# Kernel tuning notes

Measured on AMD Instinct MI355X. Metric: run time of the kernel, lower is better.

Reference implementation:

```python
import jax, jax.numpy as jnp
import numpy as np

DIM = 1024
HEADS = 16
DIM_HEAD = DIM // HEADS  # 64
B, N = 4, 1024


def setup_inputs() -> dict:
    key = jax.random.key(0)
    ks = jax.random.split(key, 8)
    s = 1.0 / np.sqrt(DIM)
    inp = {
        "x": jax.random.normal(ks[0], (B, N, DIM), dtype=jnp.float32),
        # weights stored as [in, out] so y = x @ W (+ b), equivalent to torch Linear
        "Wq": jax.random.normal(ks[1], (DIM, DIM), dtype=jnp.float32) * s,
        "Wk": jax.random.normal(ks[2], (DIM, DIM), dtype=jnp.float32) * s,
        "Wv": jax.random.normal(ks[3], (DIM, DIM), dtype=jnp.float32) * s,
        "Wproj": jax.random.normal(ks[4], (DIM, DIM), dtype=jnp.float32) * s,
        "bproj": jnp.zeros((DIM,), dtype=jnp.float32),
        "Wpre": jax.random.normal(ks[5], (DIM, DIM), dtype=jnp.float32) * s,
        "bpre": jnp.zeros((DIM,), dtype=jnp.float32),
        # original init is -inf (non-runnable); use a finite trained value
        "pi": jnp.full((1,), 0.5, dtype=jnp.float32),
    }
    return inp


def reference(x, Wq, Wk, Wv, Wproj, bproj, Wpre, bpre, pi):
    b, n, c = x.shape
    h, dh = HEADS, DIM_HEAD
    residual = x
    # bias-logit path: Linear -> SiLU -> bmm with itself (dropout p=0 is identity)
    pre = jax.nn.silu(x @ Wpre + bpre)                       # [B,N,C]
    logits = jnp.einsum('bnc,bmc->bnm', pre, pre) / jnp.sqrt(jnp.float32(c))
    # QKV (x2 defaults to x)
    q = (x @ Wq).reshape(b, n, h, dh).transpose(0, 2, 1, 3)  # [B,H,N,Dh]
    k = (x @ Wk).reshape(b, n, h, dh).transpose(0, 2, 1, 3)
    v = (x @ Wv).reshape(b, n, h, dh).transpose(0, 2, 1, 3)
    score = jnp.einsum('bhnd,bhmd->bhnm', q, k) / jnp.sqrt(jnp.float32(dh))
    final_logits = pi[0] * logits[:, None, :, :] + score     # broadcast bias over heads
    attn = jax.nn.softmax(final_logits, axis=-1)
    out = jnp.einsum('bhnm,bhmd->bhnd', attn, v)             # [B,H,N,Dh]
    out = out.transpose(0, 2, 1, 3).reshape(b, n, h * dh)
    out = out @ Wproj + bproj
    return out + residual
```

## Files before the change

kernel.cpp:

```cpp
#include <hip/hip_runtime.h>

using bf16x8 = __attribute__((ext_vector_type(8))) short;
using v8bf   = __attribute__((ext_vector_type(8))) __bf16;
using f32x4  = __attribute__((ext_vector_type(4))) float;

typedef const __attribute__((address_space(1))) void GASV;
typedef __attribute__((address_space(3))) void LASV;

template <typename V>
__device__ __forceinline__ auto mfma_bf16_impl(V a, V b, f32x4 c, int)
    -> decltype(__builtin_amdgcn_mfma_f32_16x16x32_bf16(a, b, c, 0, 0, 0)) {
  return __builtin_amdgcn_mfma_f32_16x16x32_bf16(a, b, c, 0, 0, 0);
}
template <typename V>
__device__ __forceinline__ f32x4 mfma_bf16_impl(V a, V b, f32x4 c, long) {
  return __builtin_amdgcn_mfma_f32_16x16x32_bf16(
      __builtin_bit_cast(v8bf, a), __builtin_bit_cast(v8bf, b), c, 0, 0, 0);
}
__device__ __forceinline__ f32x4 MFMA(bf16x8 a, bf16x8 b, f32x4 c) {
  return mfma_bf16_impl(a, b, c, 0);
}

__device__ __forceinline__ void async_lds16(const void* g, void* l) {
  __builtin_amdgcn_global_load_lds((GASV*)g, (LASV*)l, 16, 0, 0);
}

__device__ __forceinline__ unsigned short f2bf(float x) {
  unsigned u = __float_as_uint(x);
  u = u + 0x7fffu + ((u >> 16) & 1u);
  return (unsigned short)(u >> 16);
}

#define LOG2E 1.4426950408889634f
#define SOFT_OFF 14.0f

__global__ __launch_bounds__(256) void k_prep(
    const float4* __restrict__ x, ushort4* __restrict__ xb,
    const float* __restrict__ w0, const float* __restrict__ w1,
    const float* __restrict__ w2, const float* __restrict__ w3,
    const float* __restrict__ w4, unsigned short* __restrict__ out) {
  const int bid = blockIdx.x, tid = threadIdx.x;
  if (bid < 4096) {
    const int i = bid * 256 + tid;
    float4 v = x[i];
    ushort4 p;
    p.x = f2bf(v.x); p.y = f2bf(v.y); p.z = f2bf(v.z); p.w = f2bf(v.w);
    xb[i] = p;
    return;
  }
  __shared__ float t[32][33];
  const int tb = bid - 4096;
  const int z = tb >> 10;
  const float* W = (z == 0) ? w0 : (z == 1) ? w1 : (z == 2) ? w2 : (z == 3) ? w3 : w4;
  const float sc = (z == 1) ? (LOG2E / 8.0f) : 1.0f;
  unsigned short* o = out + (size_t)z * (1u << 20);
  const int bx = (tb & 31) * 32, by = ((tb >> 5) & 31) * 32;
  const int tx = tid & 31, ty = tid >> 5;
#pragma unroll
  for (int i = 0; i < 4; ++i)
    t[ty + i * 8][tx] = W[(size_t)(by + ty + i * 8) * 1024 + bx + tx];
  __syncthreads();
#pragma unroll
  for (int i = 0; i < 4; ++i)
    o[(size_t)(bx + ty + i * 8) * 1024 + by + tx] = f2bf(t[tx][ty + i * 8] * sc);
}

template <int MI, int NI>
__device__ __forceinline__ void gemm_core_t(const unsigned short* __restrict__ A,
                                            const unsigned short* __restrict__ Bt,
                                            unsigned short* ldsA,
                                            unsigned short* ldsB,
                                            f32x4 acc[MI][NI]) {
  const int tid = threadIdx.x;
  const int w = tid >> 6, lane = tid & 63;
  const int lane15 = lane & 15, quad = lane >> 4;
  const int wm = w >> 1, wn = w & 1;
  for (int ko = 0; ko < 16; ++ko) {
    __syncthreads();
#pragma unroll
    for (int i = 0; i < MI; ++i) {
      const int p = i * 256 + tid;
      const int r = p >> 3, cc = (p & 7) ^ (r & 7);
      async_lds16(A + r * 1024 + ko * 64 + cc * 8, ldsA + (i * 256 + w * 64) * 8);
    }
#pragma unroll
    for (int i = 0; i < NI; ++i) {
      const int p = i * 256 + tid;
      const int r = p >> 3, cc = (p & 7) ^ (r & 7);
      async_lds16(Bt + r * 1024 + ko * 64 + cc * 8, ldsB + (i * 256 + w * 64) * 8);
    }
    __syncthreads();
    bf16x8 af[MI][2], bfr[NI][2];
#pragma unroll
    for (int t = 0; t < MI; ++t) {
      const int row = wm * (MI * 16) + t * 16 + lane15;
#pragma unroll
      for (int h = 0; h < 2; ++h)
        af[t][h] = *(const bf16x8*)&ldsA[row * 64 + (((h * 4 + quad) ^ (row & 7)) << 3)];
    }
#pragma unroll
    for (int t = 0; t < NI; ++t) {
      const int row = wn * (NI * 16) + t * 16 + lane15;
#pragma unroll
      for (int h = 0; h < 2; ++h)
        bfr[t][h] = *(const bf16x8*)&ldsB[row * 64 + (((h * 4 + quad) ^ (row & 7)) << 3)];
    }
#pragma unroll
    for (int mi = 0; mi < MI; ++mi)
#pragma unroll
      for (int ni = 0; ni < NI; ++ni) {
        acc[mi][ni] = MFMA(af[mi][0], bfr[ni][0], acc[mi][ni]);
        acc[mi][ni] = MFMA(af[mi][1], bfr[ni][1], acc[mi][ni]);
      }
  }
}

#define GEMM_PROLOGUE(MI_, NI_)                                      \
  __shared__ unsigned short ldsA[(MI_)*32 * 64];                     \
  __shared__ unsigned short ldsB[(NI_)*32 * 64];                     \
  f32x4 acc[MI_][NI_];                                               \
  {                                                                  \
    f32x4 z_ = {0.f, 0.f, 0.f, 0.f};                                 \
    for (int i_ = 0; i_ < (MI_); ++i_)                               \
      for (int j_ = 0; j_ < (NI_); ++j_) acc[i_][j_] = z_;           \
  }

#define GEMM_EPI_IDX(MI_, NI_)                                       \
  const int tid = threadIdx.x, w = tid >> 6, lane = tid & 63;        \
  const int lane15 = lane & 15, quad = lane >> 4;                    \
  const int wm = w >> 1, wn = w & 1;                                 \
  const int r0 = tm + wm * ((MI_)*16) + quad * 4;                    \
  const int c0 = tn + wn * ((NI_)*16) + lane15;

__global__ __launch_bounds__(256) void k_gemm_qkvpre(
    const unsigned short* __restrict__ xb, const unsigned short* __restrict__ wt,
    const float* __restrict__ bpre, unsigned short* __restrict__ pre,
    unsigned short* __restrict__ qb, unsigned short* __restrict__ kb,
    unsigned short* __restrict__ vt) {
  const int bid = blockIdx.x;
  const int xcd = bid & 7, idx = bid >> 3;
  const int z = xcd >> 1, half = xcd & 1;
  const int wtile = (idx >> 4) * 128;
  const int stile = half * 2048 + (idx & 15) * 128;
  int tm, tn;
  if (z == 3) { tm = stile; tn = wtile; }
  else        { tm = wtile; tn = stile; }
  const unsigned short* At =
      (z == 3) ? xb + (size_t)tm * 1024
               : wt + (size_t)z * (1u << 20) + (size_t)tm * 1024;
  const unsigned short* Bt_ =
      (z == 3) ? wt + (size_t)3 * (1u << 20) + (size_t)tn * 1024
               : xb + (size_t)tn * 1024;
  GEMM_PROLOGUE(4, 4);
  gemm_core_t<4, 4>(At, Bt_, ldsA, ldsB, acc);
  GEMM_EPI_IDX(4, 4);
  if (z == 0) {
#pragma unroll
    for (int mi = 0; mi < 4; ++mi) {
      const float4 b4 = *(const float4*)&bpre[r0 + mi * 16];
#pragma unroll
      for (int ni = 0; ni < 4; ++ni) {
        const int seq = c0 + ni * 16;
        float vv[4];
#pragma unroll
        for (int rr = 0; rr < 4; ++rr) {
          float v = acc[mi][ni][rr] + ((const float*)&b4)[rr];
          vv[rr] = v / (1.0f + __expf(-v));
        }
        ushort4 pk;
        pk.x = f2bf(vv[0]); pk.y = f2bf(vv[1]);
        pk.z = f2bf(vv[2]); pk.w = f2bf(vv[3]);
        *(ushort4*)&pre[(size_t)seq * 1024 + r0 + mi * 16] = pk;
      }
    }
  } else if (z == 1 || z == 2) {
    unsigned short* dst = (z == 1) ? qb : kb;
#pragma unroll
    for (int mi = 0; mi < 4; ++mi)
#pragma unroll
      for (int ni = 0; ni < 4; ++ni) {
        const int seq = c0 + ni * 16;
        ushort4 pk;
        pk.x = f2bf(acc[mi][ni][0]); pk.y = f2bf(acc[mi][ni][1]);
        pk.z = f2bf(acc[mi][ni][2]); pk.w = f2bf(acc[mi][ni][3]);
        *(ushort4*)&dst[(size_t)seq * 1024 + r0 + mi * 16] = pk;
      }
  } else {
#pragma unroll
    for (int mi = 0; mi < 4; ++mi) {
      const int m = r0 + mi * 16;
      const int bb_ = m >> 10, nseq = m & 1023;
#pragma unroll
      for (int ni = 0; ni < 4; ++ni) {
        const int cg = c0 + ni * 16;
        const int hh = cg >> 6, dd = cg & 63;
        ushort4 pk;
        pk.x = f2bf(acc[mi][ni][0]); pk.y = f2bf(acc[mi][ni][1]);
        pk.z = f2bf(acc[mi][ni][2]); pk.w = f2bf(acc[mi][ni][3]);
        *(ushort4*)&vt[(size_t)(((bb_ * 16 + hh) << 6) + dd) * 1024 + nseq] = pk;
      }
    }
  }
}

__global__ __launch_bounds__(256) void k_gemm_logits(
    const unsigned short* __restrict__ pre, const float* __restrict__ pi,
    unsigned short* __restrict__ lg) {
  const int bz = blockIdx.z;
  const unsigned short* base = pre + ((size_t)bz << 20);
  const int tm = blockIdx.y * 64, tn = blockIdx.x * 128;
  GEMM_PROLOGUE(2, 4);
  gemm_core_t<2, 4>(base + (size_t)tm * 1024, base + (size_t)tn * 1024, ldsA, ldsB, acc);
  const float sc = pi[0] * (LOG2E / 32.0f);
  GEMM_EPI_IDX(2, 4);
#pragma unroll
  for (int mi = 0; mi < 2; ++mi)
#pragma unroll
    for (int ni = 0; ni < 4; ++ni) {
      const int col = c0 + ni * 16;
      ushort4 pk;
      pk.x = f2bf(acc[mi][ni][0] * sc); pk.y = f2bf(acc[mi][ni][1] * sc);
      pk.z = f2bf(acc[mi][ni][2] * sc); pk.w = f2bf(acc[mi][ni][3] * sc);
      *(ushort4*)&lg[((size_t)bz << 20) + (size_t)col * 1024 + r0 + mi * 16] = pk;
    }
}

__global__ __launch_bounds__(256) void k_gemm_out(
    const unsigned short* __restrict__ ao, const unsigned short* __restrict__ wtp,
    const float* __restrict__ bproj, const float* __restrict__ xres,
    float* __restrict__ out) {
  const int tm = blockIdx.x * 64, tn = blockIdx.y * 128;
  GEMM_PROLOGUE(2, 4);
  gemm_core_t<2, 4>(wtp + (size_t)tm * 1024, ao + (size_t)tn * 1024, ldsA, ldsB, acc);
  GEMM_EPI_IDX(2, 4);
#pragma unroll
  for (int mi = 0; mi < 2; ++mi) {
    const float4 b4 = *(const float4*)&bproj[r0 + mi * 16];
#pragma unroll
    for (int ni = 0; ni < 4; ++ni) {
      const int seq = c0 + ni * 16;
      const size_t idx = (size_t)seq * 1024 + r0 + mi * 16;
      const float4 rv = *(const float4*)&xres[idx];
      float4 ov;
      ov.x = acc[mi][ni][0] + b4.x + rv.x;
      ov.y = acc[mi][ni][1] + b4.y + rv.y;
      ov.z = acc[mi][ni][2] + b4.z + rv.z;
      ov.w = acc[mi][ni][3] + b4.w + rv.w;
      *(float4*)&out[idx] = ov;
    }
  }
}

__global__ __launch_bounds__(256, 5) void k_attn(
    const unsigned short* __restrict__ qb, const unsigned short* __restrict__ kb,
    const unsigned short* __restrict__ vt, const unsigned short* __restrict__ lg,
    unsigned short* __restrict__ ao) {
  __shared__ unsigned short ldsK[128 * 64];
  __shared__ unsigned short ldsV[64 * 128];
  const int bid = blockIdx.x;
  const int xcd = bid & 7, idx = bid >> 3;
  const int b = xcd >> 1, hg = xcd & 1;
  const int h = hg * 8 + (idx >> 4);
  const int q0 = (idx & 15) * 64;
  const int tid = threadIdx.x, w = tid >> 6, lane = tid & 63;
  const int lane15 = lane & 15, quad = lane >> 4;
  const int qw = q0 + w * 16;
  const int src0 = (quad & 1) * 32 + lane15;
  const int src1 = src0 + 16;
  const bool hiq = quad >= 2;

  bf16x8 qf[2];
  {
    const unsigned short* qrow =
        qb + (size_t)((b << 10) + qw + lane15) * 1024 + (h << 6);
    qf[0] = *(const bf16x8*)(qrow + quad * 8);
    qf[1] = *(const bf16x8*)(qrow + 32 + quad * 8);
  }
  float lcol = 0.f;
  f32x4 o[4];
  {
    f32x4 z_ = {0.f, 0.f, 0.f, 0.f};
#pragma unroll
    for (int nt = 0; nt < 4; ++nt) o[nt] = z_;
  }

  for (int c = 0; c < 8; ++c) {
    const int kv0 = c * 128;
    __syncthreads();
#pragma unroll
    for (int i = 0; i < 4; ++i) {
      const int p = i * 256 + tid;
      {
        const int r = p >> 3, cc = (p & 7) ^ (r & 7);
        async_lds16(kb + (size_t)((b << 10) + kv0 + r) * 1024 + (h << 6) + cc * 8,
                    ldsK + (i * 256 + w * 64) * 8);
      }
      {
        const int r = p >> 4, cc = (p & 15) ^ (r & 15);
        async_lds16(vt + (size_t)(((b * 16 + h) << 6) + r) * 1024 + kv0 + cc * 8,
                    ldsV + (i * 256 + w * 64) * 8);
      }
    }
    uint2 lgv[8];
    {
      const unsigned short* lgrow =
          lg + ((size_t)b << 20) + (size_t)(qw + lane15) * 1024 + kv0 + quad * 4;
#pragma unroll
      for (int mi = 0; mi < 8; ++mi) lgv[mi] = *(const uint2*)(lgrow + mi * 16);
    }
    __syncthreads();

    f32x4 s[8];
#pragma unroll
    for (int mi = 0; mi < 8; ++mi) {
      const int row = mi * 16 + lane15;
      bf16x8 k0 = *(const bf16x8*)&ldsK[row * 64 + ((quad ^ (row & 7)) << 3)];
      bf16x8 k1 = *(const bf16x8*)&ldsK[row * 64 + (((4 + quad) ^ (row & 7)) << 3)];
      f32x4 t;
      t[0] = __uint_as_float(lgv[mi].x << 16);
      t[1] = __uint_as_float(lgv[mi].x & 0xffff0000u);
      t[2] = __uint_as_float(lgv[mi].y << 16);
      t[3] = __uint_as_float(lgv[mi].y & 0xffff0000u);
      t = MFMA(k0, qf[0], t);
      t = MFMA(k1, qf[1], t);
      s[mi] = t;
    }
    float rs = 0.f;
    uint2 pk[8];
#pragma unroll
    for (int mi = 0; mi < 8; ++mi) {
      const float p0 = exp2f(s[mi][0] - SOFT_OFF), p1 = exp2f(s[mi][1] - SOFT_OFF);
      const float p2 = exp2f(s[mi][2] - SOFT_OFF), p3 = exp2f(s[mi][3] - SOFT_OFF);
      rs += (p0 + p1) + (p2 + p3);
      pk[mi].x = ((__float_as_uint(p1) + 0x8000u) & 0xffff0000u) |
                 ((__float_as_uint(p0) + 0x8000u) >> 16);
      pk[mi].y = ((__float_as_uint(p3) + 0x8000u) & 0xffff0000u) |
                 ((__float_as_uint(p2) + 0x8000u) >> 16);
    }
    lcol += rs;

#pragma unroll
    for (int kp = 0; kp < 4; ++kp) {
      const unsigned x0a = __shfl(pk[2 * kp].x, src0);
      const unsigned y0a = __shfl(pk[2 * kp].y, src0);
      const unsigned x1a = __shfl(pk[2 * kp].x, src1);
      const unsigned y1a = __shfl(pk[2 * kp].y, src1);
      const unsigned x0b = __shfl(pk[2 * kp + 1].x, src0);
      const unsigned y0b = __shfl(pk[2 * kp + 1].y, src0);
      const unsigned x1b = __shfl(pk[2 * kp + 1].x, src1);
      const unsigned y1b = __shfl(pk[2 * kp + 1].y, src1);
      uint4 bfv;
      bfv.x = hiq ? x0b : x0a;
      bfv.y = hiq ? y0b : y0a;
      bfv.z = hiq ? x1b : x1a;
      bfv.w = hiq ? y1b : y1a;
      const bf16x8 pf = __builtin_bit_cast(bf16x8, bfv);
#pragma unroll
      for (int dt = 0; dt < 4; ++dt) {
        const int d = dt * 16 + lane15;
        bf16x8 vf = *(const bf16x8*)&ldsV[d * 128 +
                                          (((kp * 4 + quad) ^ (d & 15)) << 3)];
        o[dt] = MFMA(vf, pf, o[dt]);
      }
    }
  }
  lcol += __shfl_xor(lcol, 16);
  lcol += __shfl_xor(lcol, 32);
  const float rinv = 1.0f / lcol;
  const int m = (b << 10) + qw + lane15;
#pragma unroll
  for (int dt = 0; dt < 4; ++dt) {
    ushort4 pkk;
    pkk.x = f2bf(o[dt][0] * rinv);
    pkk.y = f2bf(o[dt][1] * rinv);
    pkk.z = f2bf(o[dt][2] * rinv);
    pkk.w = f2bf(o[dt][3] * rinv);
    *(ushort4*)&ao[(size_t)m * 1024 + (h << 6) + dt * 16 + quad * 4] = pkk;
  }
}

extern "C" void kernel_launch(void* const* d_in, const int* in_sizes, int n_in,
                              void* d_out, int out_size, void* d_ws, size_t ws_size,
                              hipStream_t stream) {
  const float* x     = (const float*)d_in[0];
  const float* Wq    = (const float*)d_in[1];
  const float* Wk    = (const float*)d_in[2];
  const float* Wv    = (const float*)d_in[3];
  const float* Wproj = (const float*)d_in[4];
  const float* bproj = (const float*)d_in[5];
  const float* Wpre  = (const float*)d_in[6];
  const float* bpre  = (const float*)d_in[7];
  const float* pi    = (const float*)d_in[8];
  float* out = (float*)d_out;
  char* ws = (char*)d_ws;

  unsigned short* xb  = (unsigned short*)(ws);
  unsigned short* wt  = (unsigned short*)(ws + (8u << 20));
  unsigned short* pre = (unsigned short*)(ws + (18u << 20));
  unsigned short* qb  = (unsigned short*)(ws + (26u << 20));
  unsigned short* kb  = (unsigned short*)(ws + (34u << 20));
  unsigned short* vt  = (unsigned short*)(ws + (42u << 20));
  unsigned short* lg  = xb;
  unsigned short* ao  = pre;

  k_prep<<<dim3(4096 + 5120), dim3(256), 0, stream>>>(
      (const float4*)x, (ushort4*)xb, Wpre, Wq, Wk, Wv, Wproj, wt);
  k_gemm_qkvpre<<<dim3(1024), dim3(256), 0, stream>>>(xb, wt, bpre, pre, qb, kb, vt);
  k_gemm_logits<<<dim3(8, 16, 4), dim3(256), 0, stream>>>(pre, pi, lg);
  k_attn<<<dim3(1024), dim3(256), 0, stream>>>(qb, kb, vt, lg, ao);
  k_gemm_out<<<dim3(16, 32, 1), dim3(256), 0, stream>>>(ao, wt + 4 * (1u << 20), bproj, x, out);
}
```

Baseline: 234.6 us.

## Double-buffer K/V LDS tiles in attention kernel with 64-wide chunks

Splits the attention KV loop into 64-key chunks and double-buffers the K and V LDS tiles and the bias-logit registers. The next chunk's async loads are issued before computing on the current one, which hides global-to-LDS latency instead of waiting behind a sync. It also raises wave priority around the MFMA sections and lowers the occupancy hint from 5 to 4 blocks. In exchange there are twice as many chunk iterations and barriers, and possibly lower occupancy.

```diff
diff --git a/kernel.cpp b/kernel.cpp
--- a/kernel.cpp
+++ b/kernel.cpp
@@ -251,12 +251,12 @@
   }
 }
 
-__global__ __launch_bounds__(256, 5) void k_attn(
+__global__ __launch_bounds__(256, 4) void k_attn(
     const unsigned short* __restrict__ qb, const unsigned short* __restrict__ kb,
     const unsigned short* __restrict__ vt, const unsigned short* __restrict__ lg,
     unsigned short* __restrict__ ao) {
-  __shared__ unsigned short ldsK[128 * 64];
-  __shared__ unsigned short ldsV[64 * 128];
+  __shared__ unsigned short ldsK[2 * 64 * 64];
+  __shared__ unsigned short ldsV[2 * 64 * 64];
   const int bid = blockIdx.x;
   const int xcd = bid & 7, idx = bid >> 3;
   const int b = xcd >> 1, hg = xcd & 1;
@@ -276,6 +276,11 @@
     qf[0] = *(const bf16x8*)(qrow + quad * 8);
     qf[1] = *(const bf16x8*)(qrow + 32 + quad * 8);
   }
+  const unsigned short* kbase = kb + ((size_t)(b << 10)) * 1024 + (h << 6);
+  const unsigned short* vbase = vt + ((size_t)((b * 16 + h) << 6)) * 1024;
+  const unsigned short* lgrow =
+      lg + ((size_t)b << 20) + (size_t)(qw + lane15) * 1024 + quad * 4;
+
   float lcol = 0.f;
   f32x4 o[4];
   {
@@ -284,51 +289,47 @@
     for (int nt = 0; nt < 4; ++nt) o[nt] = z_;
   }
 
-  for (int c = 0; c < 8; ++c) {
-    const int kv0 = c * 128;
-    __syncthreads();
-#pragma unroll
-    for (int i = 0; i < 4; ++i) {
+  uint2 lgc[4], lgn[4];
+
+  auto stage = [&](int ch, unsigned short* sK, unsigned short* sV) {
+    const int kv0 = ch * 64;
+#pragma unroll
+    for (int i = 0; i < 2; ++i) {
       const int p = i * 256 + tid;
-      {
-        const int r = p >> 3, cc = (p & 7) ^ (r & 7);
-        async_lds16(kb + (size_t)((b << 10) + kv0 + r) * 1024 + (h << 6) + cc * 8,
-                    ldsK + (i * 256 + w * 64) * 8);
-      }
-      {
-        const int r = p >> 4, cc = (p & 15) ^ (r & 15);
-        async_lds16(vt + (size_t)(((b * 16 + h) << 6) + r) * 1024 + kv0 + cc * 8,
-                    ldsV + (i * 256 + w * 64) * 8);
-      }
-    }
-    uint2 lgv[8];
-    {
-      const unsigned short* lgrow =
-          lg + ((size_t)b << 20) + (size_t)(qw + lane15) * 1024 + kv0 + quad * 4;
-#pragma unroll
-      for (int mi = 0; mi < 8; ++mi) lgv[mi] = *(const uint2*)(lgrow + mi * 16);
-    }
-    __syncthreads();
-
-    f32x4 s[8];
-#pragma unroll
-    for (int mi = 0; mi < 8; ++mi) {
+      const int r = p >> 3, cc = (p & 7) ^ (r & 7);
+      async_lds16(kbase + (size_t)(kv0 + r) * 1024 + cc * 8,
+                  sK + (i * 256 + w * 64) * 8);
+      async_lds16(vbase + (size_t)r * 1024 + kv0 + cc * 8,
+                  sV + (i * 256 + w * 64) * 8);
+    }
+  };
+  auto lgload = [&](int ch, uint2 dst[4]) {
+#pragma unroll
+    for (int mi = 0; mi < 4; ++mi)
+      dst[mi] = *(const uint2*)(lgrow + ch * 64 + mi * 16);
+  };
+  auto compute = [&](const unsigned short* sK, const unsigned short* sV) {
+    f32x4 s[4];
+    __builtin_amdgcn_s_setprio(1);
+#pragma unroll
+    for (int mi = 0; mi < 4; ++mi) {
       const int row = mi * 16 + lane15;
-      bf16x8 k0 = *(const bf16x8*)&ldsK[row * 64 + ((quad ^ (row & 7)) << 3)];
-      bf16x8 k1 = *(const bf16x8*)&ldsK[row * 64 + (((4 + quad) ^ (row & 7)) << 3)];
+      bf16x8 k0 = *(const bf16x8*)&sK[row * 64 + ((quad ^ (row & 7)) << 3)];
+      bf16x8 k1 = *(const bf16x8*)&sK[row * 64 + (((4 + quad) ^ (row & 7)) << 3)];
       f32x4 t;
-      t[0] = __uint_as_float(lgv[mi].x << 16);
-      t[1] = __uint_as_float(lgv[mi].x & 0xffff0000u);
-      t[2] = __uint_as_float(lgv[mi].y << 16);
-      t[3] = __uint_as_float(lgv[mi].y & 0xffff0000u);
+      t[0] = __uint_as_float(lgc[mi].x << 16);
+      t[1] = __uint_as_float(lgc[mi].x & 0xffff0000u);
+      t[2] = __uint_as_float(lgc[mi].y << 16);
+      t[3] = __uint_as_float(lgc[mi].y & 0xffff0000u);
       t = MFMA(k0, qf[0], t);
       t = MFMA(k1, qf[1], t);
       s[mi] = t;
     }
+    __builtin_amdgcn_s_setprio(0);
     float rs = 0.f;
-    uint2 pk[8];
-#pragma unroll
-    for (int mi = 0; mi < 8; ++mi) {
+    uint2 pk[4];
+#pragma unroll
+    for (int mi = 0; mi < 4; ++mi) {
       const float p0 = exp2f(s[mi][0] - SOFT_OFF), p1 = exp2f(s[mi][1] - SOFT_OFF);
       const float p2 = exp2f(s[mi][2] - SOFT_OFF), p3 = exp2f(s[mi][3] - SOFT_OFF);
       rs += (p0 + p1) + (p2 + p3);
@@ -340,7 +341,7 @@
     lcol += rs;
 
 #pragma unroll
-    for (int kp = 0; kp < 4; ++kp) {
+    for (int kp = 0; kp < 2; ++kp) {
       const unsigned x0a = __shfl(pk[2 * kp].x, src0);
       const unsigned y0a = __shfl(pk[2 * kp].y, src0);
       const unsigned x1a = __shfl(pk[2 * kp].x, src1);
@@ -355,15 +356,44 @@
       bfv.z = hiq ? x1b : x1a;
       bfv.w = hiq ? y1b : y1a;
       const bf16x8 pf = __builtin_bit_cast(bf16x8, bfv);
+      __builtin_amdgcn_s_setprio(1);
 #pragma unroll
       for (int dt = 0; dt < 4; ++dt) {
         const int d = dt * 16 + lane15;
-        bf16x8 vf = *(const bf16x8*)&ldsV[d * 128 +
-                                          (((kp * 4 + quad) ^ (d & 15)) << 3)];
+        bf16x8 vf = *(const bf16x8*)&sV[d * 64 +
+                                        (((kp * 4 + quad) ^ (d & 7)) << 3)];
         o[dt] = MFMA(vf, pf, o[dt]);
       }
-    }
-  }
+      __builtin_amdgcn_s_setprio(0);
+    }
+  };
+
+  unsigned short* sK0 = ldsK;
+  unsigned short* sK1 = ldsK + 64 * 64;
+  unsigned short* sV0 = ldsV;
+  unsigned short* sV1 = ldsV + 64 * 64;
+
+  stage(0, sK0, sV0);
+  lgload(0, lgc);
+  __syncthreads();
+
+  for (int c = 0; c < 16; c += 2) {
+    stage(c + 1, sK1, sV1);
+    lgload(c + 1, lgn);
+    compute(sK0, sV0);
+    __syncthreads();
+#pragma unroll
+    for (int mi = 0; mi < 4; ++mi) lgc[mi] = lgn[mi];
+    if (c + 2 < 16) {
+      stage(c + 2, sK0, sV0);
+      lgload(c + 2, lgn);
+    }
+    compute(sK1, sV1);
+    __syncthreads();
+#pragma unroll
+    for (int mi = 0; mi < 4; ++mi) lgc[mi] = lgn[mi];
+  }
+
   lcol += __shfl_xor(lcol, 16);
   lcol += __shfl_xor(lcol, 32);
   const float rinv = 1.0f / lcol;
```

New measurement: 224.2 us. -4.4%, faster.
